# Kernel tuning notes

Hardware: AMD Instinct MI355X
Metric: run time of the kernel (lower is better)

The kernel has to match this reference:

```python
import jax, jax.numpy as jnp
import numpy as np

NUM_ITEMS = 200000
EMBED_DIM = 128
EPS = 1e-8  # torch cosine_similarity eps
TEMP = 0.1


def setup_inputs() -> dict:
    key = jax.random.key(0)
    k1, k2, k3, k4, k5, k6, k7, k8 = jax.random.split(key, 8)
    g1 = jax.random.normal(k1, (NUM_ITEMS, EMBED_DIM), dtype=jnp.float32)
    g2 = jax.random.normal(k2, (NUM_ITEMS, EMBED_DIM), dtype=jnp.float32)
    s1 = jax.random.normal(k3, (NUM_ITEMS, EMBED_DIM), dtype=jnp.float32)
    s2 = jax.random.normal(k4, (NUM_ITEMS, EMBED_DIM), dtype=jnp.float32)
    att_w = jax.random.normal(k5, (2 * EMBED_DIM,), dtype=jnp.float32)
    idx = jnp.arange(NUM_ITEMS, dtype=jnp.int32)
    # negative index != i, uniform over remaining items (matches resample loop)
    def neg(k):
        off = jax.random.randint(k, (NUM_ITEMS,), 1, NUM_ITEMS, dtype=jnp.int32)
        return (idx + off) % NUM_ITEMS
    return {
        "g_emb_1": g1, "g_emb_2": g2, "s_emb_1": s1, "s_emb_2": s2,
        "att_w": att_w,
        "neg_graph": neg(k6), "neg_seq": neg(k7), "neg_cross": neg(k8),
    }


def _cos(a, b):
    # rowwise cosine similarity with torch-style eps clamp on norm product
    num = jnp.sum(a * b, axis=-1)
    na = jnp.linalg.norm(a, axis=-1)
    nb = jnp.linalg.norm(b, axis=-1)
    return num / jnp.maximum(na * nb, EPS)


def _info_nce(e1, e2, neg_idx, temperature=TEMP):
    pos = _cos(e1, e2)                 # [N]
    neg = _cos(e1, e2[neg_idx])        # [N]
    # -log(exp(p/t)/(exp(p/t)+exp(n/t))) == softplus((n-p)/t)
    return jnp.mean(jax.nn.softplus((neg - pos) / temperature))


def reference(g_emb_1, g_emb_2, s_emb_1, s_emb_2, att_w,
              neg_graph, neg_seq, neg_cross):
    L_graph = _info_nce(g_emb_1, g_emb_2, neg_graph)
    L_seq = _info_nce(s_emb_1, s_emb_2, neg_seq)
    g_avg = 0.5 * (g_emb_1 + g_emb_2)
    s_avg = 0.5 * (s_emb_1 + s_emb_2)
    L_cross = _info_nce(g_avg, s_avg, neg_cross)
    L_CL = L_graph + L_seq + 1.0 * L_cross  # cross_weight = 1.0
    combined = jnp.concatenate([g_avg, s_avg], axis=1)  # [N, 2D]
    alpha = jax.nn.sigmoid(combined @ att_w)[:, None]   # [N, 1]
    item_embeddings = alpha * g_avg + (1.0 - alpha) * s_avg
    return item_embeddings, L_CL
```

## Files before the change

kernel.cpp:

```cpp
#include <hip/hip_runtime.h>

#define N_ITEMS 200000
#define EPSV2 1e-16f
#define INV_TEMP 10.0f

__device__ __forceinline__ float softplus_f(float x) {
    return fmaxf(x, 0.0f) + log1pf(expf(-fabsf(x)));
}

__device__ __forceinline__ float dot8(const float4& a0, const float4& a1,
                                      const float4& b0, const float4& b1) {
    return a0.x * b0.x + a0.y * b0.y + a0.z * b0.z + a0.w * b0.w +
           a1.x * b1.x + a1.y * b1.y + a1.z * b1.z + a1.w * b1.w;
}

__device__ __forceinline__ float4 avg4(const float4& a, const float4& b) {
    return make_float4(0.5f * (a.x + b.x), 0.5f * (a.y + b.y),
                       0.5f * (a.z + b.z), 0.5f * (a.w + b.w));
}

__global__ void mvr_init_ws(float* ws) {
    if (threadIdx.x < 3) ws[threadIdx.x] = 0.0f;
}

__global__ __launch_bounds__(256, 3) void mvr_main(
    const float* __restrict__ g1, const float* __restrict__ g2,
    const float* __restrict__ s1, const float* __restrict__ s2,
    const float* __restrict__ att_w,
    const int* __restrict__ neg_g, const int* __restrict__ neg_s,
    const int* __restrict__ neg_c,
    float* __restrict__ out, float* __restrict__ loss_acc)
{
    const int tid = threadIdx.x;
    const int lane = tid & 63;
    const int g = lane >> 4;
    const int l = lane & 15;
    const int wavesPerBlock = blockDim.x >> 6;
    const int waveId = blockIdx.x * wavesPerBlock + (tid >> 6);
    const int waveStride = gridDim.x * wavesPerBlock;
    const int stride4 = waveStride * 4;

    const float4* W = (const float4*)att_w;
    const float4 wa0 = W[l], wa1 = W[16 + l];
    const float4 wb0 = W[32 + l], wb1 = W[48 + l];

    const float4* G1p = (const float4*)g1;
    const float4* G2p = (const float4*)g2;
    const float4* S1p = (const float4*)s1;
    const float4* S2p = (const float4*)s2;
    float4* Op = (float4*)out;

    float accG = 0.0f, accS = 0.0f, accC = 0.0f;

    int jg, js, jc;
    {
        const int item0 = waveId * 4 + g;
        jg = neg_g[item0];
        js = neg_s[item0];
        jc = neg_c[item0];
    }

    for (int base = waveId * 4; base < N_ITEMS; base += stride4) {
        const int item = base + g;
        const size_t rb = (size_t)item * 32;
        const size_t rg = (size_t)jg * 32, rs = (size_t)js * 32, rc = (size_t)jc * 32;

        float4 G1a = G1p[rb + l], G1b = G1p[rb + 16 + l];
        float4 G2a = G2p[rb + l], G2b = G2p[rb + 16 + l];
        float4 S1a = S1p[rb + l], S1b = S1p[rb + 16 + l];
        float4 S2a = S2p[rb + l], S2b = S2p[rb + 16 + l];

        float4 Gna = G2p[rg + l], Gnb = G2p[rg + 16 + l];
        float4 Sna = S2p[rs + l], Snb = S2p[rs + 16 + l];
        float4 C1a = S1p[rc + l], C1b = S1p[rc + 16 + l];
        float4 C2a = S2p[rc + l], C2b = S2p[rc + 16 + l];

        {
            const int nbase = base + stride4;
            const int nitem = (nbase < N_ITEMS) ? (nbase + g) : item;
            jg = neg_g[nitem];
            js = neg_s[nitem];
            jc = neg_c[nitem];
        }

        __builtin_amdgcn_sched_barrier(0);

        float4 GAa = avg4(G1a, G2a), GAb = avg4(G1b, G2b);
        float4 SAa = avg4(S1a, S2a), SAb = avg4(S1b, S2b);

        float v[16];
        v[0]  = dot8(G1a, G1b, G2a, G2b);
        v[1]  = dot8(G1a, G1b, G1a, G1b);
        v[2]  = dot8(G2a, G2b, G2a, G2b);
        v[5]  = dot8(S1a, S1b, S2a, S2b);
        v[6]  = dot8(S1a, S1b, S1a, S1b);
        v[7]  = dot8(S2a, S2b, S2a, S2b);
        v[10] = dot8(GAa, GAb, SAa, SAb);
        v[11] = dot8(GAa, GAb, GAa, GAb);
        v[12] = dot8(SAa, SAb, SAa, SAb);
        v[15] = dot8(GAa, GAb, wa0, wa1) + dot8(SAa, SAb, wb0, wb1);

        __builtin_amdgcn_sched_barrier(0);

        float4 CNa = avg4(C1a, C2a), CNb = avg4(C1b, C2b);
        v[3]  = dot8(G1a, G1b, Gna, Gnb);
        v[4]  = dot8(Gna, Gnb, Gna, Gnb);
        v[8]  = dot8(S1a, S1b, Sna, Snb);
        v[9]  = dot8(Sna, Snb, Sna, Snb);
        v[13] = dot8(GAa, GAb, CNa, CNb);
        v[14] = dot8(CNa, CNb, CNa, CNb);

        #pragma unroll
        for (int off = 8; off > 0; off >>= 1) {
            #pragma unroll
            for (int k = 0; k < 16; k++)
                v[k] += __shfl_xor(v[k], off, 64);
        }

        const float cgp = v[0] * rsqrtf(fmaxf(v[1] * v[2], EPSV2));
        const float cgn = v[3] * rsqrtf(fmaxf(v[1] * v[4], EPSV2));
        accG += softplus_f((cgn - cgp) * INV_TEMP);

        const float csp = v[5] * rsqrtf(fmaxf(v[6] * v[7], EPSV2));
        const float csn = v[8] * rsqrtf(fmaxf(v[6] * v[9], EPSV2));
        accS += softplus_f((csn - csp) * INV_TEMP);

        const float ccp = v[10] * rsqrtf(fmaxf(v[11] * v[12], EPSV2));
        const float ccn = v[13] * rsqrtf(fmaxf(v[11] * v[14], EPSV2));
        accC += softplus_f((ccn - ccp) * INV_TEMP);

        const float alpha = 1.0f / (1.0f + expf(-v[15]));
        float4 o0, o1;
        o0.x = SAa.x + alpha * (GAa.x - SAa.x);
        o0.y = SAa.y + alpha * (GAa.y - SAa.y);
        o0.z = SAa.z + alpha * (GAa.z - SAa.z);
        o0.w = SAa.w + alpha * (GAa.w - SAa.w);
        o1.x = SAb.x + alpha * (GAb.x - SAb.x);
        o1.y = SAb.y + alpha * (GAb.y - SAb.y);
        o1.z = SAb.z + alpha * (GAb.z - SAb.z);
        o1.w = SAb.w + alpha * (GAb.w - SAb.w);
        Op[rb + l] = o0;
        Op[rb + 16 + l] = o1;
    }

    accG += __shfl_xor(accG, 16, 64); accG += __shfl_xor(accG, 32, 64);
    accS += __shfl_xor(accS, 16, 64); accS += __shfl_xor(accS, 32, 64);
    accC += __shfl_xor(accC, 16, 64); accC += __shfl_xor(accC, 32, 64);

    __shared__ float sh[4][3];
    const int wave = tid >> 6;
    if (lane == 0) {
        sh[wave][0] = accG;
        sh[wave][1] = accS;
        sh[wave][2] = accC;
    }
    __syncthreads();
    if (tid == 0) {
        float a = 0.0f, b = 0.0f, c = 0.0f;
        #pragma unroll
        for (int w = 0; w < 4; w++) {
            a += sh[w][0]; b += sh[w][1]; c += sh[w][2];
        }
        atomicAdd(&loss_acc[0], a);
        atomicAdd(&loss_acc[1], b);
        atomicAdd(&loss_acc[2], c);
    }
}

__global__ void mvr_finalize(const float* __restrict__ loss_acc,
                             float* __restrict__ out_scalar) {
    if (threadIdx.x == 0) {
        out_scalar[0] = (loss_acc[0] + loss_acc[1] + loss_acc[2]) * (1.0f / (float)N_ITEMS);
    }
}

extern "C" void kernel_launch(void* const* d_in, const int* in_sizes, int n_in,
                              void* d_out, int out_size, void* d_ws, size_t ws_size,
                              hipStream_t stream) {
    const float* g1    = (const float*)d_in[0];
    const float* g2    = (const float*)d_in[1];
    const float* s1    = (const float*)d_in[2];
    const float* s2    = (const float*)d_in[3];
    const float* att_w = (const float*)d_in[4];
    const int*   neg_g = (const int*)d_in[5];
    const int*   neg_s = (const int*)d_in[6];
    const int*   neg_c = (const int*)d_in[7];
    float* out = (float*)d_out;
    float* ws  = (float*)d_ws;

    mvr_init_ws<<<1, 64, 0, stream>>>(ws);
    mvr_main<<<3125, 256, 0, stream>>>(g1, g2, s1, s2, att_w,
                                       neg_g, neg_s, neg_c, out, ws);
    mvr_finalize<<<1, 64, 0, stream>>>(ws, out + (size_t)N_ITEMS * 128);
}
```

Measured before the change: 461.2 us.

## Use inline-asm vector loads with explicit waitcnt and fixed 4-item-per-wave unroll

Replaces the grid-stride loop with a fully unrolled loop of four items per wave-group at fixed 50000-item strides, and prefetches all negative indices up front. All sixteen row loads are issued as inline-asm global_load_dwordx4 with manual s_waitcnt, so the positive-pair math can start while the gathered negative rows are still in flight. It also switches to ext_vector_type arithmetic. The hardcoded grid geometry (3125 blocks × 4 waves × 4 slots × 4 items) ties correctness to the launch configuration, and the asm-volatile loads remove the compiler's freedom to schedule or merge memory operations.

Result: no change. 465.7 us (+1.0%).

```diff
diff --git a/kernel.cpp b/kernel.cpp
--- a/kernel.cpp
+++ b/kernel.cpp
@@ -4,19 +4,19 @@
 #define EPSV2 1e-16f
 #define INV_TEMP 10.0f
 
+typedef float f32x4 __attribute__((ext_vector_type(4)));
+
+#define GLOAD4(dst, ptr) \
+    asm volatile("global_load_dwordx4 %0, %1, off" : "=&v"(dst) : "v"(ptr) : "memory")
+#define WAITCNT(n) asm volatile("s_waitcnt vmcnt(" #n ")" ::: "memory")
+
 __device__ __forceinline__ float softplus_f(float x) {
     return fmaxf(x, 0.0f) + log1pf(expf(-fabsf(x)));
 }
 
-__device__ __forceinline__ float dot8(const float4& a0, const float4& a1,
-                                      const float4& b0, const float4& b1) {
-    return a0.x * b0.x + a0.y * b0.y + a0.z * b0.z + a0.w * b0.w +
-           a1.x * b1.x + a1.y * b1.y + a1.z * b1.z + a1.w * b1.w;
-}
-
-__device__ __forceinline__ float4 avg4(const float4& a, const float4& b) {
-    return make_float4(0.5f * (a.x + b.x), 0.5f * (a.y + b.y),
-                       0.5f * (a.z + b.z), 0.5f * (a.w + b.w));
+__device__ __forceinline__ float dot8(f32x4 a0, f32x4 a1, f32x4 b0, f32x4 b1) {
+    f32x4 t = a0 * b0 + a1 * b1;
+    return t.x + t.y + t.z + t.w;
 }
 
 __global__ void mvr_init_ws(float* ws) {
@@ -35,58 +35,54 @@
     const int lane = tid & 63;
     const int g = lane >> 4;
     const int l = lane & 15;
-    const int wavesPerBlock = blockDim.x >> 6;
-    const int waveId = blockIdx.x * wavesPerBlock + (tid >> 6);
-    const int waveStride = gridDim.x * wavesPerBlock;
-    const int stride4 = waveStride * 4;
+    const int waveId = blockIdx.x * 4 + (tid >> 6);
 
-    const float4* W = (const float4*)att_w;
-    const float4 wa0 = W[l], wa1 = W[16 + l];
-    const float4 wb0 = W[32 + l], wb1 = W[48 + l];
+    const f32x4* G1 = (const f32x4*)g1;
+    const f32x4* G2 = (const f32x4*)g2;
+    const f32x4* S1 = (const f32x4*)s1;
+    const f32x4* S2 = (const f32x4*)s2;
+    f32x4* Op = (f32x4*)out;
 
-    const float4* G1p = (const float4*)g1;
-    const float4* G2p = (const float4*)g2;
-    const float4* S1p = (const float4*)s1;
-    const float4* S2p = (const float4*)s2;
-    float4* Op = (float4*)out;
+    const f32x4* W = (const f32x4*)att_w;
+    const f32x4 wa0 = W[l], wa1 = W[16 + l];
+    const f32x4 wb0 = W[32 + l], wb1 = W[48 + l];
+
+    int jgs[4], jss[4], jcs[4];
+    #pragma unroll
+    for (int s = 0; s < 4; s++) {
+        const int it = waveId * 4 + s * 50000 + g;
+        jgs[s] = neg_g[it];
+        jss[s] = neg_s[it];
+        jcs[s] = neg_c[it];
+    }
 
     float accG = 0.0f, accS = 0.0f, accC = 0.0f;
 
-    int jg, js, jc;
-    {
-        const int item0 = waveId * 4 + g;
-        jg = neg_g[item0];
-        js = neg_s[item0];
-        jc = neg_c[item0];
-    }
+    #pragma unroll
+    for (int s = 0; s < 4; s++) {
+        const int item = waveId * 4 + s * 50000 + g;
+        const size_t rb = (size_t)item * 32;
+        const size_t rg = (size_t)jgs[s] * 32;
+        const size_t rs = (size_t)jss[s] * 32;
+        const size_t rc = (size_t)jcs[s] * 32;
 
-    for (int base = waveId * 4; base < N_ITEMS; base += stride4) {
-        const int item = base + g;
-        const size_t rb = (size_t)item * 32;
-        const size_t rg = (size_t)jg * 32, rs = (size_t)js * 32, rc = (size_t)jc * 32;
+        f32x4 G1a, G1b, G2a, G2b, S1a, S1b, S2a, S2b;
+        f32x4 Gna, Gnb, Sna, Snb, C1a, C1b, C2a, C2b;
 
-        float4 G1a = G1p[rb + l], G1b = G1p[rb + 16 + l];
-        float4 G2a = G2p[rb + l], G2b = G2p[rb + 16 + l];
-        float4 S1a = S1p[rb + l], S1b = S1p[rb + 16 + l];
-        float4 S2a = S2p[rb + l], S2b = S2p[rb + 16 + l];
+        GLOAD4(G1a, G1 + rb + l);  GLOAD4(G1b, G1 + rb + 16 + l);
+        GLOAD4(G2a, G2 + rb + l);  GLOAD4(G2b, G2 + rb + 16 + l);
+        GLOAD4(S1a, S1 + rb + l);  GLOAD4(S1b, S1 + rb + 16 + l);
+        GLOAD4(S2a, S2 + rb + l);  GLOAD4(S2b, S2 + rb + 16 + l);
+        GLOAD4(Gna, G2 + rg + l);  GLOAD4(Gnb, G2 + rg + 16 + l);
+        GLOAD4(Sna, S2 + rs + l);  GLOAD4(Snb, S2 + rs + 16 + l);
+        GLOAD4(C1a, S1 + rc + l);  GLOAD4(C1b, S1 + rc + 16 + l);
+        GLOAD4(C2a, S2 + rc + l);  GLOAD4(C2b, S2 + rc + 16 + l);
 
-        float4 Gna = G2p[rg + l], Gnb = G2p[rg + 16 + l];
-        float4 Sna = S2p[rs + l], Snb = S2p[rs + 16 + l];
-        float4 C1a = S1p[rc + l], C1b = S1p[rc + 16 + l];
-        float4 C2a = S2p[rc + l], C2b = S2p[rc + 16 + l];
-
-        {
-            const int nbase = base + stride4;
-            const int nitem = (nbase < N_ITEMS) ? (nbase + g) : item;
-            jg = neg_g[nitem];
-            js = neg_s[nitem];
-            jc = neg_c[nitem];
-        }
-
+        WAITCNT(8);
         __builtin_amdgcn_sched_barrier(0);
 
-        float4 GAa = avg4(G1a, G2a), GAb = avg4(G1b, G2b);
-        float4 SAa = avg4(S1a, S2a), SAb = avg4(S1b, S2b);
+        f32x4 GAa = (G1a + G2a) * 0.5f, GAb = (G1b + G2b) * 0.5f;
+        f32x4 SAa = (S1a + S2a) * 0.5f, SAb = (S1b + S2b) * 0.5f;
 
         float v[16];
         v[0]  = dot8(G1a, G1b, G2a, G2b);
@@ -100,9 +96,10 @@
         v[12] = dot8(SAa, SAb, SAa, SAb);
         v[15] = dot8(GAa, GAb, wa0, wa1) + dot8(SAa, SAb, wb0, wb1);
 
+        WAITCNT(0);
         __builtin_amdgcn_sched_barrier(0);
 
-        float4 CNa = avg4(C1a, C2a), CNb = avg4(C1b, C2b);
+        f32x4 CNa = (C1a + C2a) * 0.5f, CNb = (C1b + C2b) * 0.5f;
         v[3]  = dot8(G1a, G1b, Gna, Gnb);
         v[4]  = dot8(Gna, Gnb, Gna, Gnb);
         v[8]  = dot8(S1a, S1b, Sna, Snb);
@@ -130,15 +127,8 @@
         accC += softplus_f((ccn - ccp) * INV_TEMP);
 
         const float alpha = 1.0f / (1.0f + expf(-v[15]));
-        float4 o0, o1;
-        o0.x = SAa.x + alpha * (GAa.x - SAa.x);
-        o0.y = SAa.y + alpha * (GAa.y - SAa.y);
-        o0.z = SAa.z + alpha * (GAa.z - SAa.z);
-        o0.w = SAa.w + alpha * (GAa.w - SAa.w);
-        o1.x = SAb.x + alpha * (GAb.x - SAb.x);
-        o1.y = SAb.y + alpha * (GAb.y - SAb.y);
-        o1.z = SAb.z + alpha * (GAb.z - SAb.z);
-        o1.w = SAb.w + alpha * (GAb.w - SAb.w);
+        f32x4 o0 = SAa + alpha * (GAa - SAa);
+        f32x4 o1 = SAb + alpha * (GAb - SAb);
         Op[rb + l] = o0;
         Op[rb + 16 + l] = o1;
     }
```
